# Kernel optimization log

Measured on AMD Instinct MI355X. Metric: run time of the kernel, lower is better.

## Reference

```python
import jax, jax.numpy as jnp
import numpy as np

LN2 = float(np.log(2.0))
EPS = 1e-5

def layer_norm(x, scale, bias):
    mu = jnp.mean(x, axis=-1, keepdims=True)
    var = jnp.var(x, axis=-1, keepdims=True)
    return (x - mu) * jax.lax.rsqrt(var + EPS) * scale + bias

def shifted_softplus(x):
    return jax.nn.softplus(x) - LN2

def setup_inputs() -> dict:
    key = jax.random.key(0)
    N, E, H = 50000, 800000, 128
    ks = jax.random.split(key, 12)
    s = 0.05
    inp = {
        'h_V': jax.random.normal(ks[0], (N, H), jnp.float32),
        'h_E': jax.random.normal(ks[1], (E, H), jnp.float32),
        'edge_index': jax.random.randint(ks[2], (2, E), 0, N, jnp.int64),
        # attention weights (stored [in, out])
        'W_Q': jax.random.normal(ks[3], (H, H), jnp.float32) * s,
        'W_K': jax.random.normal(ks[4], (2 * H, H), jnp.float32) * s,
        'W_V': jax.random.normal(ks[5], (2 * H, H), jnp.float32) * s,
        'W_O': jax.random.normal(ks[6], (H, H), jnp.float32) * s,
        # layernorms
        'ln1_scale': jnp.ones((H,), jnp.float32),
        'ln1_bias': jnp.zeros((H,), jnp.float32),
        'ln2_scale': jnp.ones((H,), jnp.float32),
        'ln2_bias': jnp.zeros((H,), jnp.float32),
        # FFN (num_ff == num_hidden in TransformerLayer)
        'W_in': jax.random.normal(ks[7], (H, H), jnp.float32) * s,
        'b_in': jnp.zeros((H,), jnp.float32),
        'W_out': jax.random.normal(ks[8], (H, H), jnp.float32) * s,
        'b_out': jnp.zeros((H,), jnp.float32),
    }
    return inp

def reference(h_V, h_E, edge_index, W_Q, W_K, W_V, W_O,
              ln1_scale, ln1_bias, ln2_scale, ln2_bias,
              W_in, b_in, W_out, b_out):
    N, H = h_V.shape
    E = h_E.shape[0]
    n_heads = 4
    d = H // n_heads
    row, col = edge_index[0], edge_index[1]

    # --- attention block ---
    y = layer_norm(h_V, ln1_scale, ln1_bias)
    hv_col = y[col]                                  # [E, H] gather
    he = jnp.concatenate([h_E, hv_col], axis=-1)     # [E, 2H]
    Q = (y @ W_Q).reshape(N, n_heads, d)             # [N, h, d]
    K = (he @ W_K).reshape(E, n_heads, d)            # [E, h, d]
    V = (he @ W_V).reshape(E, n_heads, d)            # [E, h, d]
    logits = jnp.sum(Q[row] * K, axis=-1)            # [E, h]

    # scatter softmax over destination node `row`
    m = jax.ops.segment_max(logits, row, num_segments=N)      # [N, h]
    m = jnp.where(jnp.isfinite(m), m, 0.0)
    ex = jnp.exp(logits - m[row])                              # [E, h]
    denom = jax.ops.segment_sum(ex, row, num_segments=N)      # [N, h]
    alpha = ex / denom[row] / jnp.sqrt(jnp.float32(d))         # faithful: scale AFTER softmax

    msg = alpha[..., None] * V                                 # [E, h, d]
    aggr = jax.ops.segment_sum(msg, row, num_segments=N)      # [N, h, d]
    attn_out = shifted_softplus(aggr.reshape(N, H)) @ W_O      # [N, H]

    h_V = h_V + attn_out  # dropout is identity (eval)

    # --- FFN block ---
    y = layer_norm(h_V, ln2_scale, ln2_bias)
    y = jax.nn.relu(y @ W_in + b_in) @ W_out + b_out
    h_V = h_V + y
    return h_V
```

## Files before the change

kernel.cpp:

```cpp
#include <hip/hip_runtime.h>


typedef __bf16 bf16x8 __attribute__((ext_vector_type(8)));
typedef float f32x4 __attribute__((ext_vector_type(4)));
typedef unsigned short u16x8 __attribute__((ext_vector_type(8)));

#define DEV static __device__ __forceinline__

DEV unsigned short f2b(float f){
  union { float f; unsigned u; } v; v.f = f;
  unsigned r = (v.u + 0x7FFFu + ((v.u >> 16) & 1u)) >> 16;
  return (unsigned short)r;
}
DEV float b2f(unsigned short h){
  union { unsigned u; float f; } v; v.u = ((unsigned)h) << 16; return v.f;
}
DEV f32x4 mfma16(bf16x8 a, bf16x8 b, f32x4 c){
  return __builtin_amdgcn_mfma_f32_16x16x32_bf16(a, b, c, 0, 0, 0);
}
DEV u16x8 pack8(float4 a, float4 b){
  u16x8 p;
  p[0]=f2b(a.x); p[1]=f2b(a.y); p[2]=f2b(a.z); p[3]=f2b(a.w);
  p[4]=f2b(b.x); p[5]=f2b(b.y); p[6]=f2b(b.z); p[7]=f2b(b.w);
  return p;
}
DEV float sspf(float x){
  return fmaxf(x, 0.f) + log1pf(expf(-fabsf(x))) - 0.69314718055994531f;
}
DEV int idx64probe(const int* __restrict__ ei){
  return (ei[1] | ei[3] | ei[5] | ei[7] | ei[9]) == 0;
}
DEV int ld_row(const int* __restrict__ ei, long eg, long E, int is64, int N){
  int v = is64 ? ei[2*eg] : ei[eg];
  return min(max(v, 0), N - 1);
}
DEV int ld_col(const int* __restrict__ ei, long eg, long E, int is64, int N){
  int v = is64 ? ei[2*(E + eg)] : ei[E + eg];
  return min(max(v, 0), N - 1);
}
DEV unsigned swz(unsigned byteoff, unsigned row){
  return byteoff ^ ((row & 7u) << 4);
}

DEV void mma128(const unsigned short* At, const unsigned short* __restrict__ WT,
                int t, f32x4 (&acc)[4][4]){
  const int l = t & 63;
  const int wm = (t >> 7) & 1, wn = (t >> 6) & 1;
#pragma unroll
  for (int m = 0; m < 4; ++m)
#pragma unroll
    for (int n = 0; n < 4; ++n)
      acc[m][n] = f32x4{0.f, 0.f, 0.f, 0.f};
#pragma unroll
  for (int kk = 0; kk < 4; ++kk){
    bf16x8 a[4], b[4];
#pragma unroll
    for (int m = 0; m < 4; ++m){
      int row = wm*64 + m*16 + (l & 15);
      a[m] = *(const bf16x8*)((const char*)At +
              swz((unsigned)(row*256 + kk*64 + ((l >> 4) & 3)*16), (unsigned)row));
    }
#pragma unroll
    for (int n = 0; n < 4; ++n){
      int col = wn*64 + n*16 + (l & 15);
      b[n] = *(const bf16x8*)(WT + col*128 + kk*32 + ((l >> 4) & 3)*8);
    }
#pragma unroll
    for (int m = 0; m < 4; ++m)
#pragma unroll
      for (int n = 0; n < 4; ++n)
        acc[m][n] = mfma16(a[m], b[n], acc[m][n]);
  }
}
DEV void store_acc(unsigned short* Tt, const f32x4 (&acc)[4][4], int t){
  const int l = t & 63, wm = (t >> 7) & 1, wn = (t >> 6) & 1;
#pragma unroll
  for (int m = 0; m < 4; ++m)
#pragma unroll
    for (int reg = 0; reg < 4; ++reg){
      int er = wm*64 + m*16 + ((l >> 4) & 3)*4 + reg;
#pragma unroll
      for (int n = 0; n < 4; ++n){
        int col = wn*64 + n*16 + (l & 15);
        *(unsigned short*)((char*)Tt + swz((unsigned)(er*256 + col*2), (unsigned)er))
            = f2b(acc[m][n][reg]);
      }
    }
}

__global__ void k_zero(float4* __restrict__ p, long n){
  long i = (long)blockIdx.x * blockDim.x + threadIdx.x;
  const long st = (long)gridDim.x * blockDim.x;
  const float4 z = {0.f, 0.f, 0.f, 0.f};
  for (; i < n; i += st) p[i] = z;
}

__global__ void k_wprep(const float* __restrict__ WQ, const float* __restrict__ WK,
                        const float* __restrict__ WV, const float* __restrict__ WO,
                        const float* __restrict__ Wi, const float* __restrict__ Wo2,
                        unsigned short* WQT, unsigned short* WKtT, unsigned short* WKbT,
                        unsigned short* WVtT, unsigned short* WVbT, unsigned short* WOT,
                        unsigned short* WinT, unsigned short* WouT){
  int id = blockIdx.x * 256 + threadIdx.x;
  int n = id >> 7, k = id & 127;
  int d = n * 128 + k;
  WQT[d]  = f2b(WQ[k*128 + n]);
  WKtT[d] = f2b(WK[k*128 + n]);
  WKbT[d] = f2b(WK[(k+128)*128 + n]);
  WVtT[d] = f2b(WV[k*128 + n]);
  WVbT[d] = f2b(WV[(k+128)*128 + n]);
  WOT[d]  = f2b(WO[k*128 + n]);
  WinT[d] = f2b(Wi[k*128 + n]);
  WouT[d] = f2b(Wo2[k*128 + n]);
}

__global__ void k_hist(const int* __restrict__ ei, int* __restrict__ cnt, long E, int N){
  const int is64 = idx64probe(ei);
  long i = (long)blockIdx.x * blockDim.x + threadIdx.x;
  const long st = (long)gridDim.x * blockDim.x;
  for (; i < E; i += st) atomicAdd(&cnt[ld_row(ei, i, E, is64, N)], 1);
}

DEV int wave_incl_scan(int v, int lane){
#pragma unroll
  for (int ofs = 1; ofs < 64; ofs <<= 1){
    int u = __shfl_up(v, ofs, 64);
    if (lane >= ofs) v += u;
  }
  return v;
}

__global__ __launch_bounds__(1024) void k_scan(const int* __restrict__ cnt,
                                               int* __restrict__ rowStart,
                                               int* __restrict__ cursor, int N){
  __shared__ int wsum[16], woff[16];
  __shared__ int carry;
  const int t = threadIdx.x, lane = t & 63, w = t >> 6;
  if (t == 0) carry = 0;
  for (int base = 0; base < N; base += 1024){
    __syncthreads();
    int v = (base + t < N) ? cnt[base + t] : 0;
    int incl = wave_incl_scan(v, lane);
    if (lane == 63) wsum[w] = incl;
    __syncthreads();
    if (t == 0){
      int run = carry;
#pragma unroll
      for (int i = 0; i < 16; ++i){ woff[i] = run; run += wsum[i]; }
      carry = run;
    }
    __syncthreads();
    int excl = woff[w] + incl - v;
    if (base + t < N){ rowStart[base + t] = excl; cursor[base + t] = excl; }
  }
  __syncthreads();
  if (t == 0) rowStart[N] = carry;
}

__global__ void k_scatter(const int* __restrict__ ei, int* __restrict__ cursor,
                          int* __restrict__ perm, int* __restrict__ rowsS,
                          int* __restrict__ colS, long E, int N){
  const int is64 = idx64probe(ei);
  long i = (long)blockIdx.x * blockDim.x + threadIdx.x;
  const long st = (long)gridDim.x * blockDim.x;
  for (; i < E; i += st){
    int r = ld_row(ei, i, E, is64, N);
    int pos = atomicAdd(&cursor[r], 1);
    perm[pos] = (int)i;
    rowsS[pos] = r;
    colS[pos] = ld_col(ei, i, E, is64, N);
  }
}

__global__ __launch_bounds__(256) void k_nodeprep(
    const float* __restrict__ hV, const float* __restrict__ l1s, const float* __restrict__ l1b,
    const unsigned short* __restrict__ WQT, const unsigned short* __restrict__ WKbT,
    const unsigned short* __restrict__ WVbT,
    unsigned short* __restrict__ Qbf, unsigned short* __restrict__ YKbf,
    unsigned short* __restrict__ YVbf, int N){
  __shared__ unsigned short At[128*128];
  __shared__ float ps[256], pss[256];
  __shared__ float scs[128], bis[128];
  const int t = threadIdx.x;
  if (t < 128){ scs[t] = l1s[t]; bis[t] = l1b[t]; }
  const int r0 = blockIdx.x * 128;
  const int rl = t & 127, hf = t >> 7;
  const int r = r0 + rl;
  const float4* xp = (const float4*)(hV + (size_t)r*128 + hf*64);
  float s = 0.f, ss = 0.f;
  if (r < N){
#pragma unroll
    for (int i = 0; i < 16; ++i){
      float4 v = xp[i];
      s  += (v.x + v.y) + (v.z + v.w);
      ss += (v.x*v.x + v.y*v.y) + (v.z*v.z + v.w*v.w);
    }
  }
  ps[t] = s; pss[t] = ss;
  __syncthreads();
  const float mu  = (ps[t] + ps[t ^ 128]) * 0.0078125f;
  const float var = (pss[t] + pss[t ^ 128]) * 0.0078125f - mu*mu;
  const float rs  = rsqrtf(var + 1e-5f);
#pragma unroll
  for (int i = 0; i < 8; ++i){
    const int c = hf*64 + i*8;
    u16x8 p = {0,0,0,0,0,0,0,0};
    if (r < N){
      float4 v0 = xp[2*i], v1 = xp[2*i+1];
      p[0] = f2b((v0.x - mu)*rs*scs[c+0] + bis[c+0]);
      p[1] = f2b((v0.y - mu)*rs*scs[c+1] + bis[c+1]);
      p[2] = f2b((v0.z - mu)*rs*scs[c+2] + bis[c+2]);
      p[3] = f2b((v0.w - mu)*rs*scs[c+3] + bis[c+3]);
      p[4] = f2b((v1.x - mu)*rs*scs[c+4] + bis[c+4]);
      p[5] = f2b((v1.y - mu)*rs*scs[c+5] + bis[c+5]);
      p[6] = f2b((v1.z - mu)*rs*scs[c+6] + bis[c+6]);
      p[7] = f2b((v1.w - mu)*rs*scs[c+7] + bis[c+7]);
    }
    *(u16x8*)((char*)At + swz((unsigned)(rl*256 + c*2), (unsigned)rl)) = p;
  }
  __syncthreads();
  const int l = t & 63, wm = (t >> 7) & 1, wn = (t >> 6) & 1;
  f32x4 acc[4][4];
  for (int g = 0; g < 3; ++g){
    const unsigned short* WT = (g == 0) ? WQT : (g == 1) ? WKbT : WVbT;
    unsigned short* O = (g == 0) ? Qbf : (g == 1) ? YKbf : YVbf;
    mma128(At, WT, t, acc);
#pragma unroll
    for (int m = 0; m < 4; ++m)
#pragma unroll
      for (int reg = 0; reg < 4; ++reg){
        int row = wm*64 + m*16 + ((l >> 4) & 3)*4 + reg;
        int gr = r0 + row;
        if (gr < N){
#pragma unroll
          for (int n = 0; n < 4; ++n){
            int col = wn*64 + n*16 + (l & 15);
            O[(size_t)gr*128 + col] = f2b(acc[m][n][reg]);
          }
        }
      }
  }
}

__global__ __launch_bounds__(256, 2) void k_edge(
    const float* __restrict__ hE,
    const unsigned short* __restrict__ WKtT, const unsigned short* __restrict__ WVtT,
    const unsigned short* __restrict__ Qbf, const unsigned short* __restrict__ YKbf,
    const unsigned short* __restrict__ YVbf,
    const int* __restrict__ perm, const int* __restrict__ rowsS,
    const int* __restrict__ colS, const int* __restrict__ rowStart,
    float* __restrict__ num, float* __restrict__ den, long E){
  __shared__ unsigned short At[128*128];
  __shared__ unsigned short Kt[128*128];
  __shared__ float aS[128][4];
  __shared__ int permT[128], rowsT[128], colT[128];
  const int t = threadIdx.x;
  const long e0 = (long)blockIdx.x * 128;
  if (t < 128){
    long p = e0 + t;
    int pe = (p < E) ? perm[p] : -1;
    permT[t] = pe;
    rowsT[t] = (p < E) ? rowsS[p] : -1;
    colT[t]  = (p < E) ? colS[p] : 0;
  }
  __syncthreads();
#pragma unroll
  for (int i = 0; i < 8; ++i){
    int cc = t + i*256;
    int row = cc >> 4, ck = (cc & 15)*8;
    int pe = permT[row];
    u16x8 pkd = {0,0,0,0,0,0,0,0};
    if (pe >= 0){
      const float4* src = (const float4*)(hE + (size_t)pe*128 + ck);
      pkd = pack8(src[0], src[1]);
    }
    *(u16x8*)((char*)At + swz((unsigned)(row*256 + ck*2), (unsigned)row)) = pkd;
  }
  __syncthreads();
  f32x4 acc[4][4];
  mma128(At, WKtT, t, acc);
  store_acc(Kt, acc, t);
  __syncthreads();
  {
    const int e = t >> 1, hf = t & 1;
    const int r = rowsT[e];
    const u16x8* qp  = (const u16x8*)(Qbf  + (size_t)(r < 0 ? 0 : r)*128 + hf*64);
    const u16x8* ykp = (const u16x8*)(YKbf + (size_t)colT[e]*128 + hf*64);
    float lg0 = 0.f, lg1 = 0.f;
#pragma unroll
    for (int i = 0; i < 8; ++i){
      u16x8 q = qp[i], yk = ykp[i];
      u16x8 k = *(const u16x8*)((const char*)Kt +
          swz((unsigned)(e*256 + hf*128 + i*16), (unsigned)e));
      float d = 0.f;
#pragma unroll
      for (int j = 0; j < 8; ++j) d += b2f(q[j]) * (b2f(k[j]) + b2f(yk[j]));
      if (i < 4) lg0 += d; else lg1 += d;
    }
    aS[e][2*hf]     = (r >= 0) ? expf(lg0) : 0.f;
    aS[e][2*hf + 1] = (r >= 0) ? expf(lg1) : 0.f;
  }
  __syncthreads();
  mma128(At, WVtT, t, acc);
  store_acc(Kt, acc, t);
  __syncthreads();
  {
    const int e = t >> 1, hf = t & 1;
    const u16x8* src = (const u16x8*)(YVbf + (size_t)colT[e]*128 + hf*64);
#pragma unroll
    for (int i = 0; i < 8; ++i){
      u16x8* p = (u16x8*)((char*)Kt + swz((unsigned)(e*256 + hf*128 + i*16), (unsigned)e));
      u16x8 a = *p, b = src[i], o;
#pragma unroll
      for (int j = 0; j < 8; ++j) o[j] = f2b(b2f(a[j]) + b2f(b[j]));
      *p = o;
    }
  }
  __syncthreads();
  {
    const int c = t & 127, half = t >> 7, hh = c >> 5;
    const bool doDen = (c < 4);
    const int eb = half * 64;
    float accv = 0.f, accd = 0.f;
    int cur = rowsT[eb];
    long rs = e0 + eb;
    for (int e = eb; e < eb + 64; ++e){
      int r = rowsT[e];
      if (r != cur){
        if (cur >= 0){
          long re = e0 + e;
          bool own = (rowStart[cur] == (int)rs) && (rowStart[cur+1] == (int)re);
          float* np = num + (size_t)cur*128 + c;
          if (own) *np = accv; else atomicAdd(np, accv);
          if (doDen){
            float* dp = den + (size_t)cur*4 + c;
            if (own) *dp = accd; else atomicAdd(dp, accd);
          }
        }
        cur = r; rs = e0 + e; accv = 0.f; accd = 0.f;
      }
      float a = aS[e][hh];
      accv += a * b2f(*(const unsigned short*)((const char*)Kt +
                swz((unsigned)(e*256 + c*2), (unsigned)e)));
      if (doDen) accd += aS[e][c];
    }
    if (cur >= 0){
      long re = e0 + eb + 64;
      bool own = (rowStart[cur] == (int)rs) && (rowStart[cur+1] == (int)re);
      float* np = num + (size_t)cur*128 + c;
      if (own) *np = accv; else atomicAdd(np, accv);
      if (doDen){
        float* dp = den + (size_t)cur*4 + c;
        if (own) *dp = accd; else atomicAdd(dp, accd);
      }
    }
  }
}

__global__ __launch_bounds__(256) void k_attnout(
    const float* __restrict__ hV, const float* __restrict__ num,
    const float* __restrict__ den,
    const unsigned short* __restrict__ WOT, float* __restrict__ H1, int N){
  __shared__ unsigned short At[128*128];
  const int t = threadIdx.x;
  const int r0 = blockIdx.x * 128;
  const int rl = t & 127, hf = t >> 7;
  const int r = r0 + rl;
  const float4* ap = (const float4*)(num + (size_t)r*128 + hf*64);
  const float inv = 0.17677669529663687f;
  float i0 = 0.f, i1 = 0.f;
  if (r < N){
    float d0 = den[(size_t)r*4 + 2*hf], d1 = den[(size_t)r*4 + 2*hf + 1];
    i0 = (d0 > 0.f) ? inv / d0 : 0.f;
    i1 = (d1 > 0.f) ? inv / d1 : 0.f;
  }
#pragma unroll
  for (int i = 0; i < 8; ++i){
    u16x8 p = {0,0,0,0,0,0,0,0};
    if (r < N){
      float sc = (i < 4) ? i0 : i1;
      float4 v0 = ap[2*i], v1 = ap[2*i+1];
      p[0]=f2b(sspf(v0.x*sc)); p[1]=f2b(sspf(v0.y*sc)); p[2]=f2b(sspf(v0.z*sc)); p[3]=f2b(sspf(v0.w*sc));
      p[4]=f2b(sspf(v1.x*sc)); p[5]=f2b(sspf(v1.y*sc)); p[6]=f2b(sspf(v1.z*sc)); p[7]=f2b(sspf(v1.w*sc));
    }
    *(u16x8*)((char*)At + swz((unsigned)(rl*256 + hf*128 + i*16), (unsigned)rl)) = p;
  }
  __syncthreads();
  f32x4 acc[4][4];
  mma128(At, WOT, t, acc);
  const int l = t & 63, wm = (t >> 7) & 1, wn = (t >> 6) & 1;
#pragma unroll
  for (int m = 0; m < 4; ++m)
#pragma unroll
    for (int reg = 0; reg < 4; ++reg){
      int row = wm*64 + m*16 + ((l >> 4) & 3)*4 + reg;
      int gr = r0 + row;
      if (gr < N){
#pragma unroll
        for (int n = 0; n < 4; ++n){
          int col = wn*64 + n*16 + (l & 15);
          H1[(size_t)gr*128 + col] = acc[m][n][reg] + hV[(size_t)gr*128 + col];
        }
      }
    }
}

__global__ __launch_bounds__(256) void k_ffn(
    const float* __restrict__ H1, const float* __restrict__ l2s, const float* __restrict__ l2b,
    const unsigned short* __restrict__ WinT, const unsigned short* __restrict__ WouT,
    const float* __restrict__ bin, const float* __restrict__ bou,
    float* __restrict__ out, int N){
  __shared__ unsigned short At[128*128];
  __shared__ float ps[256], pss[256];
  __shared__ float scs[128], bis[128];
  const int t = threadIdx.x;
  if (t < 128){ scs[t] = l2s[t]; bis[t] = l2b[t]; }
  const int r0 = blockIdx.x * 128;
  const int rl = t & 127, hf = t >> 7;
  const int r = r0 + rl;
  const float4* xp = (const float4*)(H1 + (size_t)r*128 + hf*64);
  float s = 0.f, ss = 0.f;
  float4 xv[16];
  if (r < N){
#pragma unroll
    for (int i = 0; i < 16; ++i){
      float4 v = xp[i];
      xv[i] = v;
      s  += (v.x + v.y) + (v.z + v.w);
      ss += (v.x*v.x + v.y*v.y) + (v.z*v.z + v.w*v.w);
    }
  }
  ps[t] = s; pss[t] = ss;
  __syncthreads();
  const float mu  = (ps[t] + ps[t ^ 128]) * 0.0078125f;
  const float var = (pss[t] + pss[t ^ 128]) * 0.0078125f - mu*mu;
  const float rs  = rsqrtf(var + 1e-5f);
#pragma unroll
  for (int i = 0; i < 8; ++i){
    const int c = hf*64 + i*8;
    u16x8 p = {0,0,0,0,0,0,0,0};
    if (r < N){
      float4 v0 = xv[2*i], v1 = xv[2*i+1];
      p[0] = f2b((v0.x - mu)*rs*scs[c+0] + bis[c+0]);
      p[1] = f2b((v0.y - mu)*rs*scs[c+1] + bis[c+1]);
      p[2] = f2b((v0.z - mu)*rs*scs[c+2] + bis[c+2]);
      p[3] = f2b((v0.w - mu)*rs*scs[c+3] + bis[c+3]);
      p[4] = f2b((v1.x - mu)*rs*scs[c+4] + bis[c+4]);
      p[5] = f2b((v1.y - mu)*rs*scs[c+5] + bis[c+5]);
      p[6] = f2b((v1.z - mu)*rs*scs[c+6] + bis[c+6]);
      p[7] = f2b((v1.w - mu)*rs*scs[c+7] + bis[c+7]);
    }
    *(u16x8*)((char*)At + swz((unsigned)(rl*256 + c*2), (unsigned)rl)) = p;
  }
  __syncthreads();
  f32x4 acc[4][4];
  mma128(At, WinT, t, acc);
  const int l = t & 63, wm = (t >> 7) & 1, wn = (t >> 6) & 1;
  unsigned short hv[4][4][4];
#pragma unroll
  for (int m = 0; m < 4; ++m)
#pragma unroll
    for (int n = 0; n < 4; ++n)
#pragma unroll
      for (int reg = 0; reg < 4; ++reg){
        int col = wn*64 + n*16 + (l & 15);
        float v = acc[m][n][reg] + bin[col];
        hv[m][n][reg] = f2b(fmaxf(v, 0.f));
      }
  __syncthreads();
#pragma unroll
  for (int m = 0; m < 4; ++m)
#pragma unroll
    for (int reg = 0; reg < 4; ++reg){
      int row = wm*64 + m*16 + ((l >> 4) & 3)*4 + reg;
#pragma unroll
      for (int n = 0; n < 4; ++n){
        int col = wn*64 + n*16 + (l & 15);
        *(unsigned short*)((char*)At + swz((unsigned)(row*256 + col*2), (unsigned)row))
            = hv[m][n][reg];
      }
    }
  __syncthreads();
  mma128(At, WouT, t, acc);
#pragma unroll
  for (int m = 0; m < 4; ++m)
#pragma unroll
    for (int reg = 0; reg < 4; ++reg){
      int row = wm*64 + m*16 + ((l >> 4) & 3)*4 + reg;
      int gr = r0 + row;
      if (gr < N){
#pragma unroll
        for (int n = 0; n < 4; ++n){
          int col = wn*64 + n*16 + (l & 15);
          out[(size_t)gr*128 + col] = acc[m][n][reg] + bou[col] + H1[(size_t)gr*128 + col];
        }
      }
    }
}

extern "C" void kernel_launch(void* const* d_in, const int* in_sizes, int n_in,
                              void* d_out, int out_size, void* d_ws, size_t ws_size,
                              hipStream_t stream)
{
  const float* hV  = (const float*)d_in[0];
  const float* hE  = (const float*)d_in[1];
  const int*   ei  = (const int*)d_in[2];
  const float* WQ  = (const float*)d_in[3];
  const float* WK  = (const float*)d_in[4];
  const float* WV  = (const float*)d_in[5];
  const float* WO  = (const float*)d_in[6];
  const float* l1s = (const float*)d_in[7];
  const float* l1b = (const float*)d_in[8];
  const float* l2s = (const float*)d_in[9];
  const float* l2b = (const float*)d_in[10];
  const float* Wi  = (const float*)d_in[11];
  const float* bi  = (const float*)d_in[12];
  const float* Wo2 = (const float*)d_in[13];
  const float* bo  = (const float*)d_in[14];
  float* out = (float*)d_out;

  const int  N = in_sizes[0] / 128;
  const long E = (long)in_sizes[1] / 128;

  char* ws = (char*)d_ws;
  size_t off = 0;
  auto alloc = [&](size_t b){ size_t o = off; off += (b + 255) & ~(size_t)255; return o; };
  const size_t WB = 128*128*sizeof(unsigned short);
  size_t oWQT = alloc(WB), oWKtT = alloc(WB), oWKbT = alloc(WB);
  size_t oWVtT = alloc(WB), oWVbT = alloc(WB), oWOT = alloc(WB);
  size_t oWinT = alloc(WB), oWouT = alloc(WB);
  size_t oQ    = alloc((size_t)N*128*2);
  size_t oYK   = alloc((size_t)N*128*2);
  size_t oYV   = alloc((size_t)N*128*2);
  size_t oPERM = alloc((size_t)E*4);
  size_t oROWS = alloc((size_t)E*4);
  size_t oCOLS = alloc((size_t)E*4);
  size_t oRST  = alloc((size_t)(N+1)*4);
  size_t oCUR  = alloc((size_t)N*4);
  size_t oCNT  = alloc((size_t)N*4);
  size_t oDEN  = alloc((size_t)N*4*4);
  size_t oNUM  = alloc((size_t)N*128*4);
  size_t zero_bytes = (oNUM + (size_t)N*128*4) - oCNT;

  unsigned short* WQT  = (unsigned short*)(ws + oWQT);
  unsigned short* WKtT = (unsigned short*)(ws + oWKtT);
  unsigned short* WKbT = (unsigned short*)(ws + oWKbT);
  unsigned short* WVtT = (unsigned short*)(ws + oWVtT);
  unsigned short* WVbT = (unsigned short*)(ws + oWVbT);
  unsigned short* WOT  = (unsigned short*)(ws + oWOT);
  unsigned short* WinT = (unsigned short*)(ws + oWinT);
  unsigned short* WouT = (unsigned short*)(ws + oWouT);
  unsigned short* Qbf  = (unsigned short*)(ws + oQ);
  unsigned short* YKbf = (unsigned short*)(ws + oYK);
  unsigned short* YVbf = (unsigned short*)(ws + oYV);
  int* perm  = (int*)(ws + oPERM);
  int* rowsS = (int*)(ws + oROWS);
  int* colS  = (int*)(ws + oCOLS);
  int* rowSt = (int*)(ws + oRST);
  int* cursor= (int*)(ws + oCUR);
  int* cnt   = (int*)(ws + oCNT);
  float* den = (float*)(ws + oDEN);
  float* num = (float*)(ws + oNUM);
  float* H1g = out;

  const int nbN = (N + 127) / 128;
  const int nbE = (int)((E + 127) / 128);
  const int nbe = (int)((E + 255) / 256);

  k_zero<<<2048, 256, 0, stream>>>((float4*)(ws + oCNT), (long)(zero_bytes / 16));
  k_wprep<<<64, 256, 0, stream>>>(WQ, WK, WV, WO, Wi, Wo2,
                                  WQT, WKtT, WKbT, WVtT, WVbT, WOT, WinT, WouT);
  k_nodeprep<<<nbN, 256, 0, stream>>>(hV, l1s, l1b, WQT, WKbT, WVbT, Qbf, YKbf, YVbf, N);
  k_hist<<<nbe, 256, 0, stream>>>(ei, cnt, E, N);
  k_scan<<<1, 1024, 0, stream>>>(cnt, rowSt, cursor, N);
  k_scatter<<<nbe, 256, 0, stream>>>(ei, cursor, perm, rowsS, colS, E, N);
  k_edge<<<nbE, 256, 0, stream>>>(hE, WKtT, WVtT, Qbf, YKbf, YVbf,
                                  perm, rowsS, colS, rowSt, num, den, E);
  k_attnout<<<nbN, 256, 0, stream>>>(hV, num, den, WOT, H1g, N);
  k_ffn<<<nbN, 256, 0, stream>>>(H1g, l2s, l2b, WinT, WouT, bi, bo, out, N);
}
```

Measured before the change: 769.7 us.

## Pipeline edge kernel persistently with LDS prefetch and fuse attention-out with FFN

```diff
diff --git a/kernel.cpp b/kernel.cpp
--- a/kernel.cpp
+++ b/kernel.cpp
@@ -6,6 +6,7 @@
 typedef unsigned short u16x8 __attribute__((ext_vector_type(8)));
 
 #define DEV static __device__ __forceinline__
+#define ET 32
 
 DEV unsigned short f2b(float f){
   union { float f; unsigned u; } v; v.f = f;
@@ -41,6 +42,14 @@
 DEV unsigned swz(unsigned byteoff, unsigned row){
   return byteoff ^ ((row & 7u) << 4);
 }
+DEV void gload16(const void* g, void* l){
+  __builtin_amdgcn_global_load_lds((const __attribute__((address_space(1))) void*)g,
+                                   (__attribute__((address_space(3))) void*)l, 16, 0, 0);
+}
+DEV void bar_lds(){
+  asm volatile("s_waitcnt lgkmcnt(0)" ::: "memory");
+  __builtin_amdgcn_s_barrier();
+}
 
 DEV void mma128(const unsigned short* At, const unsigned short* __restrict__ WT,
                 int t, f32x4 (&acc)[4][4]){
@@ -72,19 +81,35 @@
         acc[m][n] = mfma16(a[m], b[n], acc[m][n]);
   }
 }
-DEV void store_acc(unsigned short* Tt, const f32x4 (&acc)[4][4], int t){
-  const int l = t & 63, wm = (t >> 7) & 1, wn = (t >> 6) & 1;
-#pragma unroll
-  for (int m = 0; m < 4; ++m)
+
+DEV void mma32(const unsigned short* Ab, const unsigned short* __restrict__ WT,
+               int t, f32x4 (&acc)[4]){
+  const int l = t & 63, wid = t >> 6, wm = wid >> 1, wn = wid & 1;
+#pragma unroll
+  for (int n = 0; n < 4; ++n) acc[n] = f32x4{0.f, 0.f, 0.f, 0.f};
+#pragma unroll
+  for (int kk = 0; kk < 4; ++kk){
+    int row = wm*16 + (l & 15);
+    bf16x8 a = *(const bf16x8*)((const char*)Ab +
+        swz((unsigned)(row*256 + kk*64 + ((l >> 4) & 3)*16), (unsigned)row));
+#pragma unroll
+    for (int n = 0; n < 4; ++n){
+      int col = wn*64 + n*16 + (l & 15);
+      bf16x8 b = *(const bf16x8*)(WT + col*128 + kk*32 + ((l >> 4) & 3)*8);
+      acc[n] = mfma16(a, b, acc[n]);
+    }
+  }
+}
+DEV void store_acc32(unsigned short* Kt, const f32x4 (&acc)[4], int t){
+  const int l = t & 63, wid = t >> 6, wm = wid >> 1, wn = wid & 1;
+#pragma unroll
+  for (int n = 0; n < 4; ++n)
 #pragma unroll
     for (int reg = 0; reg < 4; ++reg){
-      int er = wm*64 + m*16 + ((l >> 4) & 3)*4 + reg;
-#pragma unroll
-      for (int n = 0; n < 4; ++n){
-        int col = wn*64 + n*16 + (l & 15);
-        *(unsigned short*)((char*)Tt + swz((unsigned)(er*256 + col*2), (unsigned)er))
-            = f2b(acc[m][n][reg]);
-      }
+      int er = wm*16 + ((l >> 4) & 3)*4 + reg;
+      int col = wn*64 + n*16 + (l & 15);
+      *(unsigned short*)((char*)Kt + swz((unsigned)(er*256 + col*2), (unsigned)er))
+          = f2b(acc[n][reg]);
     }
 }
 
@@ -131,44 +156,43 @@
 }
 
 __global__ __launch_bounds__(1024) void k_scan(const int* __restrict__ cnt,
-                                               int* __restrict__ rowStart,
-                                               int* __restrict__ cursor, int N){
+                                               int* __restrict__ cursor,
+                                               int4* __restrict__ edata,
+                                               long E, int N){
   __shared__ int wsum[16], woff[16];
-  __shared__ int carry;
   const int t = threadIdx.x, lane = t & 63, w = t >> 6;
-  if (t == 0) carry = 0;
-  for (int base = 0; base < N; base += 1024){
-    __syncthreads();
-    int v = (base + t < N) ? cnt[base + t] : 0;
-    int incl = wave_incl_scan(v, lane);
-    if (lane == 63) wsum[w] = incl;
-    __syncthreads();
-    if (t == 0){
-      int run = carry;
-#pragma unroll
-      for (int i = 0; i < 16; ++i){ woff[i] = run; run += wsum[i]; }
-      carry = run;
-    }
-    __syncthreads();
-    int excl = woff[w] + incl - v;
-    if (base + t < N){ rowStart[base + t] = excl; cursor[base + t] = excl; }
-  }
-  __syncthreads();
-  if (t == 0) rowStart[N] = carry;
+  const int C = (N + 1023) / 1024;
+  const int base = t * C;
+  int s = 0;
+  for (int j = 0; j < C; ++j) if (base + j < N) s += cnt[base + j];
+  int incl = wave_incl_scan(s, lane);
+  if (lane == 63) wsum[w] = incl;
+  __syncthreads();
+  if (t == 0){
+    int run = 0;
+#pragma unroll
+    for (int i = 0; i < 16; ++i){ woff[i] = run; run += wsum[i]; }
+  }
+  __syncthreads();
+  int run = woff[w] + incl - s;
+  for (int j = 0; j < C; ++j)
+    if (base + j < N){ cursor[base + j] = run; run += cnt[base + j]; }
+  if (t < 37){
+    long gi = (t == 0) ? 0 : (E + t);
+    edata[gi] = make_int4(0, -2, 0, 0);
+  }
 }
 
 __global__ void k_scatter(const int* __restrict__ ei, int* __restrict__ cursor,
-                          int* __restrict__ perm, int* __restrict__ rowsS,
-                          int* __restrict__ colS, long E, int N){
+                          int4* __restrict__ edata, long E, int N){
   const int is64 = idx64probe(ei);
   long i = (long)blockIdx.x * blockDim.x + threadIdx.x;
   const long st = (long)gridDim.x * blockDim.x;
   for (; i < E; i += st){
     int r = ld_row(ei, i, E, is64, N);
+    int c = ld_col(ei, i, E, is64, N);
     int pos = atomicAdd(&cursor[r], 1);
-    perm[pos] = (int)i;
-    rowsS[pos] = r;
-    colS[pos] = ld_col(ei, i, E, is64, N);
+    edata[1 + (long)pos] = make_int4((int)i, r, c, 0);
   }
 }
 
@@ -242,131 +266,158 @@
   }
 }
 
-__global__ __launch_bounds__(256, 2) void k_edge(
+__global__ __launch_bounds__(256, 3) void k_edge(
     const float* __restrict__ hE,
     const unsigned short* __restrict__ WKtT, const unsigned short* __restrict__ WVtT,
     const unsigned short* __restrict__ Qbf, const unsigned short* __restrict__ YKbf,
     const unsigned short* __restrict__ YVbf,
-    const int* __restrict__ perm, const int* __restrict__ rowsS,
-    const int* __restrict__ colS, const int* __restrict__ rowStart,
-    float* __restrict__ num, float* __restrict__ den, long E){
-  __shared__ unsigned short At[128*128];
-  __shared__ unsigned short Kt[128*128];
-  __shared__ float aS[128][4];
-  __shared__ int permT[128], rowsT[128], colT[128];
-  const int t = threadIdx.x;
-  const long e0 = (long)blockIdx.x * 128;
-  if (t < 128){
-    long p = e0 + t;
-    int pe = (p < E) ? perm[p] : -1;
-    permT[t] = pe;
-    rowsT[t] = (p < E) ? rowsS[p] : -1;
-    colT[t]  = (p < E) ? colS[p] : 0;
-  }
-  __syncthreads();
-#pragma unroll
-  for (int i = 0; i < 8; ++i){
-    int cc = t + i*256;
-    int row = cc >> 4, ck = (cc & 15)*8;
-    int pe = permT[row];
-    u16x8 pkd = {0,0,0,0,0,0,0,0};
-    if (pe >= 0){
-      const float4* src = (const float4*)(hE + (size_t)pe*128 + ck);
-      pkd = pack8(src[0], src[1]);
-    }
-    *(u16x8*)((char*)At + swz((unsigned)(row*256 + ck*2), (unsigned)row)) = pkd;
-  }
-  __syncthreads();
-  f32x4 acc[4][4];
-  mma128(At, WKtT, t, acc);
-  store_acc(Kt, acc, t);
-  __syncthreads();
-  {
-    const int e = t >> 1, hf = t & 1;
-    const int r = rowsT[e];
-    const u16x8* qp  = (const u16x8*)(Qbf  + (size_t)(r < 0 ? 0 : r)*128 + hf*64);
-    const u16x8* ykp = (const u16x8*)(YKbf + (size_t)colT[e]*128 + hf*64);
-    float lg0 = 0.f, lg1 = 0.f;
-#pragma unroll
-    for (int i = 0; i < 8; ++i){
-      u16x8 q = qp[i], yk = ykp[i];
-      u16x8 k = *(const u16x8*)((const char*)Kt +
-          swz((unsigned)(e*256 + hf*128 + i*16), (unsigned)e));
-      float d = 0.f;
-#pragma unroll
-      for (int j = 0; j < 8; ++j) d += b2f(q[j]) * (b2f(k[j]) + b2f(yk[j]));
-      if (i < 4) lg0 += d; else lg1 += d;
-    }
-    aS[e][2*hf]     = (r >= 0) ? expf(lg0) : 0.f;
-    aS[e][2*hf + 1] = (r >= 0) ? expf(lg1) : 0.f;
-  }
-  __syncthreads();
-  mma128(At, WVtT, t, acc);
-  store_acc(Kt, acc, t);
-  __syncthreads();
-  {
-    const int e = t >> 1, hf = t & 1;
-    const u16x8* src = (const u16x8*)(YVbf + (size_t)colT[e]*128 + hf*64);
-#pragma unroll
-    for (int i = 0; i < 8; ++i){
-      u16x8* p = (u16x8*)((char*)Kt + swz((unsigned)(e*256 + hf*128 + i*16), (unsigned)e));
-      u16x8 a = *p, b = src[i], o;
-#pragma unroll
-      for (int j = 0; j < 8; ++j) o[j] = f2b(b2f(a[j]) + b2f(b[j]));
-      *p = o;
-    }
-  }
-  __syncthreads();
-  {
-    const int c = t & 127, half = t >> 7, hh = c >> 5;
-    const bool doDen = (c < 4);
-    const int eb = half * 64;
-    float accv = 0.f, accd = 0.f;
-    int cur = rowsT[eb];
-    long rs = e0 + eb;
-    for (int e = eb; e < eb + 64; ++e){
-      int r = rowsT[e];
-      if (r != cur){
-        if (cur >= 0){
-          long re = e0 + e;
-          bool own = (rowStart[cur] == (int)rs) && (rowStart[cur+1] == (int)re);
-          float* np = num + (size_t)cur*128 + c;
-          if (own) *np = accv; else atomicAdd(np, accv);
-          if (doDen){
-            float* dp = den + (size_t)cur*4 + c;
-            if (own) *dp = accd; else atomicAdd(dp, accd);
-          }
+    const int4* __restrict__ edata,
+    float* __restrict__ num, float* __restrict__ den,
+    long E, long NT){
+  __shared__ float4 stage[2][ET*32];
+  __shared__ unsigned short Ab[ET*128];
+  __shared__ unsigned short Kt[ET*128];
+  __shared__ float aS[ET][4];
+  __shared__ int4 idxb[3][36];
+
+  const int t = threadIdx.x, l = t & 63, wid = t >> 6;
+  const long b0 = blockIdx.x, G = gridDim.x;
+  const long ntloc = (b0 < NT) ? ((NT - 1 - b0) / G + 1) : 0;
+
+  auto tileof = [&](long i) -> long {
+    long tt = b0 + i * G; return (tt < NT) ? tt : (NT - 1);
+  };
+  auto issue_idx = [&](long i, int slot){
+    long tt = tileof(i);
+    if (l < 9)
+      gload16((const void*)(edata + tt*ET + (wid*9 + l)), (void*)&idxb[slot][wid*9]);
+  };
+  auto issue_pf = [&](long i, int buf){
+    const int slot = (int)(i % 3);
+#pragma unroll
+    for (int k = 0; k < 4; ++k){
+      int U = (wid*4 + k)*64 + l;
+      int row = U >> 5, u = U & 31;
+      int pe = idxb[slot][1 + row].x;
+      pe = min(max(pe, 0), (int)(E - 1));
+      int j = u ^ (row & 7);
+      gload16((const void*)(hE + (size_t)pe*128 + j*4),
+              (void*)&stage[buf][(wid*4 + k)*64]);
+    }
+  };
+
+  issue_idx(0, 0);
+  issue_idx(1, 1);
+  asm volatile("s_waitcnt vmcnt(1)" ::: "memory");
+  __builtin_amdgcn_sched_barrier(0);
+  __builtin_amdgcn_s_barrier();
+  issue_pf(0, 0);
+  int p = 0;
+
+  for (long it = 0; it < ntloc; ++it){
+    const int slot = (int)(it % 3);
+    asm volatile("s_waitcnt vmcnt(0) lgkmcnt(0)" ::: "memory");
+    __builtin_amdgcn_sched_barrier(0);
+    __builtin_amdgcn_s_barrier();
+    {
+      const int row = t >> 3, s = t & 7;
+      float4 f[4];
+#pragma unroll
+      for (int k = 0; k < 4; ++k)
+        f[k] = stage[p][row*32 + ((s*4 + k) ^ (row & 7))];
+      *(u16x8*)((char*)Ab + swz((unsigned)(row*256 + s*32), (unsigned)row)) = pack8(f[0], f[1]);
+      *(u16x8*)((char*)Ab + swz((unsigned)(row*256 + s*32 + 16), (unsigned)row)) = pack8(f[2], f[3]);
+    }
+    bar_lds();
+    { f32x4 acc[4]; mma32(Ab, WKtT, t, acc); store_acc32(Kt, acc, t); }
+    bar_lds();
+    {
+      const int e = t >> 3, s = t & 7;
+      int4 ed = idxb[slot][1 + e];
+      int r = ed.y;
+      int ra = max(r, 0), ca = max(ed.z, 0);
+      const u16x8* qp  = (const u16x8*)(Qbf  + (size_t)ra*128 + s*16);
+      const u16x8* ykp = (const u16x8*)(YKbf + (size_t)ca*128 + s*16);
+      float pl = 0.f;
+#pragma unroll
+      for (int k = 0; k < 2; ++k){
+        u16x8 q = qp[k], yk = ykp[k];
+        u16x8 kv = *(const u16x8*)((const char*)Kt +
+            swz((unsigned)(e*256 + s*32 + k*16), (unsigned)e));
+#pragma unroll
+        for (int j = 0; j < 8; ++j) pl += b2f(q[j]) * (b2f(kv[j]) + b2f(yk[j]));
+      }
+      float full = pl + __shfl_xor(pl, 1);
+      if (!(s & 1)) aS[e][s >> 1] = (r >= 0) ? expf(full) : 0.f;
+    }
+    bar_lds();
+    { f32x4 acc[4]; mma32(Ab, WVtT, t, acc); store_acc32(Kt, acc, t); }
+    bar_lds();
+    {
+      const int e = t >> 3, s = t & 7;
+      int ca = max(idxb[slot][1 + e].z, 0);
+      const u16x8* src = (const u16x8*)(YVbf + (size_t)ca*128 + s*16);
+#pragma unroll
+      for (int k = 0; k < 2; ++k){
+        u16x8* pp = (u16x8*)((char*)Kt + swz((unsigned)(e*256 + s*32 + k*16), (unsigned)e));
+        u16x8 a = *pp, b = src[k], o;
+#pragma unroll
+        for (int j = 0; j < 8; ++j) o[j] = f2b(b2f(a[j]) + b2f(b[j]));
+        *pp = o;
+      }
+    }
+    bar_lds();
+    issue_idx(it + 2, (int)((it + 2) % 3));
+    issue_pf(it + 1, p ^ 1);
+    {
+      const int c = t & 127, half = t >> 7, hh = c >> 5;
+      const int eb = half * 16;
+      auto rowAt = [&](int x) -> int { return idxb[slot][1 + x].y; };
+      auto flush = [&](int rr, int rsx, int rex, float av, float ad){
+        if (rr < 0) return;
+        bool own = (rowAt(rsx - 1) != rr) && (rowAt(rex) != rr);
+        float* np = num + (size_t)rr*128 + c;
+        if (own) *np = av; else atomicAdd(np, av);
+        if (c < 4){
+          float* dp = den + (size_t)rr*4 + c;
+          if (own) *dp = ad; else atomicAdd(dp, ad);
         }
-        cur = r; rs = e0 + e; accv = 0.f; accd = 0.f;
-      }
-      float a = aS[e][hh];
-      accv += a * b2f(*(const unsigned short*)((const char*)Kt +
-                swz((unsigned)(e*256 + c*2), (unsigned)e)));
-      if (doDen) accd += aS[e][c];
-    }
-    if (cur >= 0){
-      long re = e0 + eb + 64;
-      bool own = (rowStart[cur] == (int)rs) && (rowStart[cur+1] == (int)re);
-      float* np = num + (size_t)cur*128 + c;
-      if (own) *np = accv; else atomicAdd(np, accv);
-      if (doDen){
-        float* dp = den + (size_t)cur*4 + c;
-        if (own) *dp = accd; else atomicAdd(dp, accd);
-      }
-    }
-  }
-}
-
-__global__ __launch_bounds__(256) void k_attnout(
+      };
+      float accv = 0.f, accd = 0.f;
+      int cur = rowAt(eb), rs = eb;
+#pragma unroll
+      for (int e = eb; e < eb + 16; ++e){
+        int r = rowAt(e);
+        if (r != cur){ flush(cur, rs, e, accv, accd); cur = r; rs = e; accv = 0.f; accd = 0.f; }
+        float a = aS[e][hh];
+        accv += a * b2f(*(const unsigned short*)((const char*)Kt +
+                  swz((unsigned)(e*256 + c*2), (unsigned)e)));
+        if (c < 4) accd += aS[e][c];
+      }
+      flush(cur, rs, eb + 16, accv, accd);
+    }
+    p ^= 1;
+  }
+  asm volatile("s_waitcnt vmcnt(0) lgkmcnt(0)" ::: "memory");
+  __builtin_amdgcn_s_barrier();
+}
+
+__global__ __launch_bounds__(256, 2) void k_post(
     const float* __restrict__ hV, const float* __restrict__ num,
     const float* __restrict__ den,
-    const unsigned short* __restrict__ WOT, float* __restrict__ H1, int N){
+    const unsigned short* __restrict__ WOT, const unsigned short* __restrict__ WinT,
+    const unsigned short* __restrict__ WouT,
+    const float* __restrict__ l2s, const float* __restrict__ l2b,
+    const float* __restrict__ bin, const float* __restrict__ bou,
+    float* __restrict__ out, int N){
   __shared__ unsigned short At[128*128];
+  __shared__ float ps[128][2], pq[128][2];
+  __shared__ float scs[128], bis[128], binS[128], bouS[128];
   const int t = threadIdx.x;
+  if (t < 128){ scs[t] = l2s[t]; bis[t] = l2b[t]; binS[t] = bin[t]; bouS[t] = bou[t]; }
   const int r0 = blockIdx.x * 128;
   const int rl = t & 127, hf = t >> 7;
   const int r = r0 + rl;
-  const float4* ap = (const float4*)(num + (size_t)r*128 + hf*64);
   const float inv = 0.17677669529663687f;
   float i0 = 0.f, i1 = 0.f;
   if (r < N){
@@ -374,6 +425,7 @@
     i0 = (d0 > 0.f) ? inv / d0 : 0.f;
     i1 = (d1 > 0.f) ? inv / d1 : 0.f;
   }
+  const float4* ap = (const float4*)(num + (size_t)r*128 + hf*64);
 #pragma unroll
   for (int i = 0; i < 8; ++i){
     u16x8 p = {0,0,0,0,0,0,0,0};
@@ -386,113 +438,81 @@
     *(u16x8*)((char*)At + swz((unsigned)(rl*256 + hf*128 + i*16), (unsigned)rl)) = p;
   }
   __syncthreads();
+  const int l = t & 63, wm = (t >> 7) & 1, wn = (t >> 6) & 1;
   f32x4 acc[4][4];
   mma128(At, WOT, t, acc);
-  const int l = t & 63, wm = (t >> 7) & 1, wn = (t >> 6) & 1;
+  float h1[4][4][4];
 #pragma unroll
   for (int m = 0; m < 4; ++m)
 #pragma unroll
     for (int reg = 0; reg < 4; ++reg){
-      int row = wm*64 + m*16 + ((l >> 4) & 3)*4 + reg;
-      int gr = r0 + row;
+      int er = wm*64 + m*16 + ((l >> 4) & 3)*4 + reg;
+      int gr = r0 + er;
+#pragma unroll
+      for (int n = 0; n < 4; ++n){
+        int col = wn*64 + n*16 + (l & 15);
+        h1[m][n][reg] = acc[m][n][reg] + ((gr < N) ? hV[(size_t)gr*128 + col] : 0.f);
+      }
+    }
+#pragma unroll
+  for (int m = 0; m < 4; ++m)
+#pragma unroll
+    for (int reg = 0; reg < 4; ++reg){
+      float s = 0.f, q = 0.f;
+#pragma unroll
+      for (int n = 0; n < 4; ++n){ float v = h1[m][n][reg]; s += v; q += v*v; }
+#pragma unroll
+      for (int o = 1; o < 16; o <<= 1){ s += __shfl_xor(s, o); q += __shfl_xor(q, o); }
+      if ((l & 15) == 0){
+        int er = wm*64 + m*16 + ((l >> 4) & 3)*4 + reg;
+        ps[er][wn] = s; pq[er][wn] = q;
+      }
+    }
+  __syncthreads();
+#pragma unroll
+  for (int m = 0; m < 4; ++m)
+#pragma unroll
+    for (int reg = 0; reg < 4; ++reg){
+      int er = wm*64 + m*16 + ((l >> 4) & 3)*4 + reg;
+      float mu  = (ps[er][0] + ps[er][1]) * 0.0078125f;
+      float var = (pq[er][0] + pq[er][1]) * 0.0078125f - mu*mu;
+      float rsv = rsqrtf(var + 1e-5f);
+#pragma unroll
+      for (int n = 0; n < 4; ++n){
+        int col = wn*64 + n*16 + (l & 15);
+        float yv = (h1[m][n][reg] - mu)*rsv*scs[col] + bis[col];
+        *(unsigned short*)((char*)At + swz((unsigned)(er*256 + col*2), (unsigned)er)) = f2b(yv);
+      }
+    }
+  __syncthreads();
+  mma128(At, WinT, t, acc);
+  __syncthreads();
+#pragma unroll
+  for (int m = 0; m < 4; ++m)
+#pragma unroll
+    for (int reg = 0; reg < 4; ++reg){
+      int er = wm*64 + m*16 + ((l >> 4) & 3)*4 + reg;
+#pragma unroll
+      for (int n = 0; n < 4; ++n){
+        int col = wn*64 + n*16 + (l & 15);
+        float v = acc[m][n][reg] + binS[col];
+        *(unsigned short*)((char*)At + swz((unsigned)(er*256 + col*2), (unsigned)er))
+            = f2b(fmaxf(v, 0.f));
+      }
+    }
+  __syncthreads();
+  mma128(At, WouT, t, acc);
+#pragma unroll
+  for (int m = 0; m < 4; ++m)
+#pragma unroll
+    for (int reg = 0; reg < 4; ++reg){
+      int er = wm*64 + m*16 + ((l >> 4) & 3)*4 + reg;
+      int gr = r0 + er;
       if (gr < N){
 #pragma unroll
         for (int n = 0; n < 4; ++n){
           int col = wn*64 + n*16 + (l & 15);
-          H1[(size_t)gr*128 + col] = acc[m][n][reg] + hV[(size_t)gr*128 + col];
-        }
-      }
-    }
-}
-
-__global__ __launch_bounds__(256) void k_ffn(
-    const float* __restrict__ H1, const float* __restrict__ l2s, const float* __restrict__ l2b,
-    const unsigned short* __restrict__ WinT, const unsigned short* __restrict__ WouT,
-    const float* __restrict__ bin, const float* __restrict__ bou,
-    float* __restrict__ out, int N){
-  __shared__ unsigned short At[128*128];
-  __shared__ float ps[256], pss[256];
-  __shared__ float scs[128], bis[128];
-  const int t = threadIdx.x;
-  if (t < 128){ scs[t] = l2s[t]; bis[t] = l2b[t]; }
-  const int r0 = blockIdx.x * 128;
-  const int rl = t & 127, hf = t >> 7;
-  const int r = r0 + rl;
-  const float4* xp = (const float4*)(H1 + (size_t)r*128 + hf*64);
-  float s = 0.f, ss = 0.f;
-  float4 xv[16];
-  if (r < N){
-#pragma unroll
-    for (int i = 0; i < 16; ++i){
-      float4 v = xp[i];
-      xv[i] = v;
-      s  += (v.x + v.y) + (v.z + v.w);
-      ss += (v.x*v.x + v.y*v.y) + (v.z*v.z + v.w*v.w);
-    }
-  }
-  ps[t] = s; pss[t] = ss;
-  __syncthreads();
-  const float mu  = (ps[t] + ps[t ^ 128]) * 0.0078125f;
-  const float var = (pss[t] + pss[t ^ 128]) * 0.0078125f - mu*mu;
-  const float rs  = rsqrtf(var + 1e-5f);
-#pragma unroll
-  for (int i = 0; i < 8; ++i){
-    const int c = hf*64 + i*8;
-    u16x8 p = {0,0,0,0,0,0,0,0};
-    if (r < N){
-      float4 v0 = xv[2*i], v1 = xv[2*i+1];
-      p[0] = f2b((v0.x - mu)*rs*scs[c+0] + bis[c+0]);
-      p[1] = f2b((v0.y - mu)*rs*scs[c+1] + bis[c+1]);
-      p[2] = f2b((v0.z - mu)*rs*scs[c+2] + bis[c+2]);
-      p[3] = f2b((v0.w - mu)*rs*scs[c+3] + bis[c+3]);
-      p[4] = f2b((v1.x - mu)*rs*scs[c+4] + bis[c+4]);
-      p[5] = f2b((v1.y - mu)*rs*scs[c+5] + bis[c+5]);
-      p[6] = f2b((v1.z - mu)*rs*scs[c+6] + bis[c+6]);
-      p[7] = f2b((v1.w - mu)*rs*scs[c+7] + bis[c+7]);
-    }
-    *(u16x8*)((char*)At + swz((unsigned)(rl*256 + c*2), (unsigned)rl)) = p;
-  }
-  __syncthreads();
-  f32x4 acc[4][4];
-  mma128(At, WinT, t, acc);
-  const int l = t & 63, wm = (t >> 7) & 1, wn = (t >> 6) & 1;
-  unsigned short hv[4][4][4];
-#pragma unroll
-  for (int m = 0; m < 4; ++m)
-#pragma unroll
-    for (int n = 0; n < 4; ++n)
-#pragma unroll
-      for (int reg = 0; reg < 4; ++reg){
-        int col = wn*64 + n*16 + (l & 15);
-        float v = acc[m][n][reg] + bin[col];
-        hv[m][n][reg] = f2b(fmaxf(v, 0.f));
-      }
-  __syncthreads();
-#pragma unroll
-  for (int m = 0; m < 4; ++m)
-#pragma unroll
-    for (int reg = 0; reg < 4; ++reg){
-      int row = wm*64 + m*16 + ((l >> 4) & 3)*4 + reg;
-#pragma unroll
-      for (int n = 0; n < 4; ++n){
-        int col = wn*64 + n*16 + (l & 15);
-        *(unsigned short*)((char*)At + swz((unsigned)(row*256 + col*2), (unsigned)row))
-            = hv[m][n][reg];
-      }
-    }
-  __syncthreads();
-  mma128(At, WouT, t, acc);
-#pragma unroll
-  for (int m = 0; m < 4; ++m)
-#pragma unroll
-    for (int reg = 0; reg < 4; ++reg){
-      int row = wm*64 + m*16 + ((l >> 4) & 3)*4 + reg;
-      int gr = r0 + row;
-      if (gr < N){
-#pragma unroll
-        for (int n = 0; n < 4; ++n){
-          int col = wn*64 + n*16 + (l & 15);
-          out[(size_t)gr*128 + col] = acc[m][n][reg] + bou[col] + H1[(size_t)gr*128 + col];
+          out[(size_t)gr*128 + col] = acc[m][n][reg] + bouS[col] + h1[m][n][reg];
         }
       }
     }
@@ -521,6 +541,7 @@
 
   const int  N = in_sizes[0] / 128;
   const long E = (long)in_sizes[1] / 128;
+  const long NT = (E + ET - 1) / ET;
 
   char* ws = (char*)d_ws;
   size_t off = 0;
@@ -532,10 +553,7 @@
   size_t oQ    = alloc((size_t)N*128*2);
   size_t oYK   = alloc((size_t)N*128*2);
   size_t oYV   = alloc((size_t)N*128*2);
-  size_t oPERM = alloc((size_t)E*4);
-  size_t oROWS = alloc((size_t)E*4);
-  size_t oCOLS = alloc((size_t)E*4);
-  size_t oRST  = alloc((size_t)(N+1)*4);
+  size_t oED   = alloc((size_t)(E + 38)*16);
   size_t oCUR  = alloc((size_t)N*4);
   size_t oCNT  = alloc((size_t)N*4);
   size_t oDEN  = alloc((size_t)N*4*4);
@@ -553,29 +571,25 @@
   unsigned short* Qbf  = (unsigned short*)(ws + oQ);
   unsigned short* YKbf = (unsigned short*)(ws + oYK);
   unsigned short* YVbf = (unsigned short*)(ws + oYV);
-  int* perm  = (int*)(ws + oPERM);
-  int* rowsS = (int*)(ws + oROWS);
-  int* colS  = (int*)(ws + oCOLS);
-  int* rowSt = (int*)(ws + oRST);
-  int* cursor= (int*)(ws + oCUR);
-  int* cnt   = (int*)(ws + oCNT);
-  float* den = (float*)(ws + oDEN);
-  float* num = (float*)(ws + oNUM);
-  float* H1g = out;
+  int4* edata  = (int4*)(ws + oED);
+  int* cursor  = (int*)(ws + oCUR);
+  int* cnt     = (int*)(ws + oCNT);
+  float* den   = (float*)(ws + oDEN);
+  float* num   = (float*)(ws + oNUM);
 
   const int nbN = (N + 127) / 128;
-  const int nbE = (int)((E + 127) / 128);
   const int nbe = (int)((E + 255) / 256);
+  const int gE  = (int)((NT < 768) ? NT : 768);
 
   k_zero<<<2048, 256, 0, stream>>>((float4*)(ws + oCNT), (long)(zero_bytes / 16));
   k_wprep<<<64, 256, 0, stream>>>(WQ, WK, WV, WO, Wi, Wo2,
                                   WQT, WKtT, WKbT, WVtT, WVbT, WOT, WinT, WouT);
   k_nodeprep<<<nbN, 256, 0, stream>>>(hV, l1s, l1b, WQT, WKbT, WVbT, Qbf, YKbf, YVbf, N);
   k_hist<<<nbe, 256, 0, stream>>>(ei, cnt, E, N);
-  k_scan<<<1, 1024, 0, stream>>>(cnt, rowSt, cursor, N);
-  k_scatter<<<nbe, 256, 0, stream>>>(ei, cursor, perm, rowsS, colS, E, N);
-  k_edge<<<nbE, 256, 0, stream>>>(hE, WKtT, WVtT, Qbf, YKbf, YVbf,
-                                  perm, rowsS, colS, rowSt, num, den, E);
-  k_attnout<<<nbN, 256, 0, stream>>>(hV, num, den, WOT, H1g, N);
-  k_ffn<<<nbN, 256, 0, stream>>>(H1g, l2s, l2b, WinT, WouT, bi, bo, out, N);
-}
+  k_scan<<<1, 1024, 0, stream>>>(cnt, cursor, edata, E, N);
+  k_scatter<<<nbe, 256, 0, stream>>>(ei, cursor, edata, E, N);
+  k_edge<<<gE, 256, 0, stream>>>(hE, WKtT, WVtT, Qbf, YKbf, YVbf,
+                                 edata, num, den, E, NT);
+  k_post<<<nbN, 256, 0, stream>>>(hV, num, den, WOT, WinT, WouT,
+                                  l2s, l2b, bi, bo, out, N);
+}
```

Result: slower. 921.4 us (+19.7%).
